# Performance work log

Hardware: AMD Instinct MI355X
Metric: run time of the kernel (lower is better)

The kernel has to match this reference:

```python
import jax, jax.numpy as jnp
import numpy as np

DIM = 1024
NUM_HEADS = 16
HEAD_DIM = DIM // NUM_HEADS
EPS = 1e-5


def layernorm(x, scale, bias):
    # LayerNorm over the last (head_dim) axis
    mu = jnp.mean(x, axis=-1, keepdims=True)
    var = jnp.var(x, axis=-1, keepdims=True)
    return (x - mu) * jax.lax.rsqrt(var + EPS) * scale + bias


def rope(q):
    # q: [B, H, S, Hd]; standard rotate-half RoPE over head_dim
    S, Hd = q.shape[-2], q.shape[-1]
    inv_freq = 1.0 / (10000.0 ** (jnp.arange(0, Hd, 2, dtype=jnp.float32) / Hd))
    ang = jnp.arange(S, dtype=jnp.float32)[:, None] * inv_freq  # [S, Hd/2]
    cos, sin = jnp.cos(ang), jnp.sin(ang)
    q1, q2 = jnp.split(q, 2, axis=-1)
    return jnp.concatenate([q1 * cos - q2 * sin, q1 * sin + q2 * cos], axis=-1)


def setup_inputs() -> dict:
    key = jax.random.key(0)
    ks = jax.random.split(key, 8)
    B, S, S_ctx = 4, 2048, 2048
    s = 0.02
    return {
        "x": jax.random.normal(ks[0], (B, S, DIM), dtype=jnp.float32),
        "context": jax.random.normal(ks[1], (B, S_ctx, DIM), dtype=jnp.float32),
        "q_w": jax.random.normal(ks[2], (DIM, DIM), dtype=jnp.float32) * s,
        "kv_w": jax.random.normal(ks[3], (DIM, 2 * DIM), dtype=jnp.float32) * s,
        "qn_scale": jnp.ones((HEAD_DIM,), jnp.float32),
        "qn_bias": jnp.zeros((HEAD_DIM,), jnp.float32),
        "kn_scale": jnp.ones((HEAD_DIM,), jnp.float32),
        "kn_bias": jnp.zeros((HEAD_DIM,), jnp.float32),
        "proj_w": jax.random.normal(ks[4], (DIM, DIM), dtype=jnp.float32) * s,
        "proj_b": jnp.zeros((DIM,), jnp.float32),
    }


def reference(x, context, q_w, kv_w, qn_scale, qn_bias, kn_scale, kn_bias, proj_w, proj_b):
    B, S, C = x.shape
    S_ctx = context.shape[1]
    H, Hd = NUM_HEADS, HEAD_DIM
    # projections (no bias: qkv_bias=False)
    q = (x @ q_w).reshape(B, S, H, Hd).transpose(0, 2, 1, 3)        # [B,H,S,Hd]
    kv = (context @ kv_w).reshape(B, S_ctx, 2, H, Hd)
    k = kv[:, :, 0].transpose(0, 2, 1, 3)                           # [B,H,Sc,Hd]
    v = kv[:, :, 1].transpose(0, 2, 1, 3)
    # per-head LayerNorm on q and k
    q = layernorm(q, qn_scale, qn_bias)
    k = layernorm(k, kn_scale, kn_bias)
    # RoPE on q only (as in the original forward)
    q = rope(q)
    # SDPA (eval path: no mask, no dropout)
    scale = 1.0 / jnp.sqrt(jnp.float32(Hd))
    logits = jnp.einsum("bhsd,bhtd->bhst", q, k) * scale
    attn = jax.nn.softmax(logits, axis=-1)
    out = jnp.einsum("bhst,bhtd->bhsd", attn, v)                    # [B,H,S,Hd]
    out = out.transpose(0, 2, 1, 3).reshape(B, S, C)
    return out @ proj_w + proj_b
```

## Files before the change

kernel.cpp:

```cpp
#include <hip/hip_runtime.h>
#include <hip/hip_bf16.h>


typedef short bf16x8 __attribute__((ext_vector_type(8)));
typedef float f32x4 __attribute__((ext_vector_type(4)));

__device__ __forceinline__ short f2s(float f) {
    __hip_bfloat16 h = __float2bfloat16(f);
    return __builtin_bit_cast(short, h);
}

__device__ __forceinline__ f32x4 mfma16(bf16x8 a, bf16x8 b, f32x4 c) {
    return __builtin_amdgcn_mfma_f32_16x16x32_bf16(a, b, c, 0, 0, 0);
}

__device__ __forceinline__ void gload16(short* lds, const short* g) {
    __builtin_amdgcn_global_load_lds((const __attribute__((address_space(1))) void*)g,
                                     (__attribute__((address_space(3))) void*)lds,
                                     16, 0, 0);
}

__device__ __forceinline__ void drain_barrier() {
    asm volatile("s_waitcnt vmcnt(0) lgkmcnt(0)" ::: "memory");
    __syncthreads();
}

__device__ __forceinline__ unsigned int fbits(float f) {
    return __builtin_bit_cast(unsigned int, f);
}

__global__ __launch_bounds__(256) void conv_to_bf16(const float* __restrict__ x,
                                                    const float* __restrict__ ctx,
                                                    short* __restrict__ xb,
                                                    short* __restrict__ cb) {
    const size_t NV = 2097152;
    size_t i = (size_t)blockIdx.x * 256 + threadIdx.x;
    const float4* src = (i < NV) ? (const float4*)x : (const float4*)ctx;
    short* dst = (i < NV) ? xb : cb;
    size_t idx = (i < NV) ? i : i - NV;
    float4 v = src[idx];
    short4 o;
    o.x = f2s(v.x); o.y = f2s(v.y); o.z = f2s(v.z); o.w = f2s(v.w);
    ((short4*)dst)[idx] = o;
}

__global__ __launch_bounds__(256) void transpose_weights(
    const float* __restrict__ q_w, const float* __restrict__ kv_w,
    const float* __restrict__ proj_w,
    short* __restrict__ WqT, short* __restrict__ WkvT, short* __restrict__ WpT) {
    __shared__ float t[32][33];
    const float* src; short* dst; int ld, coff;
    switch (blockIdx.z) {
        case 0:  src = q_w;    dst = WqT;                 ld = 1024; coff = 0;    break;
        case 1:  src = kv_w;   dst = WkvT;                ld = 2048; coff = 0;    break;
        case 2:  src = kv_w;   dst = WkvT + 1024 * 1024;  ld = 2048; coff = 1024; break;
        default: src = proj_w; dst = WpT;                 ld = 1024; coff = 0;    break;
    }
    int n0 = blockIdx.x * 32, k0 = blockIdx.y * 32;
    int tx = threadIdx.x & 31, ty = threadIdx.x >> 5;
    #pragma unroll
    for (int j = 0; j < 32; j += 8)
        t[ty + j][tx] = src[(size_t)(k0 + ty + j) * ld + coff + n0 + tx];
    __syncthreads();
    #pragma unroll
    for (int j = 0; j < 32; j += 8)
        dst[(size_t)(n0 + ty + j) * 1024 + k0 + tx] = f2s(t[tx][ty + j]);
}

template <int MODE>
__global__ __launch_bounds__(256, 3) void gemm128(
    const short* __restrict__ A,
    const short* __restrict__ Bt,
    const short* __restrict__ A2,
    const short* __restrict__ Bt2,
    const float* __restrict__ qn_scale, const float* __restrict__ qn_bias,
    const float* __restrict__ kn_scale, const float* __restrict__ kn_bias,
    short* __restrict__ outQ, short* __restrict__ outK, short* __restrict__ outV,
    float* __restrict__ outF, const float* __restrict__ bias_vec) {
    __shared__ short smem[24576];
    const int tid = threadIdx.x;
    const int w = tid >> 6, lane = tid & 63, quad = lane >> 4, l15 = lane & 15;
    const int wr = w & 1, wc = w >> 1;
    const int m0 = blockIdx.x * 128;

    int n0;
    bool qpath = true, vpath = false;
    const short *Ab, *Bb;
    const float *lns = qn_scale, *lnb = qn_bias;
    if constexpr (MODE == 3) {
        const int y = blockIdx.y;
        qpath = (y < 8);
        n0 = qpath ? y * 128 : (y - 8) * 128;
        Ab = qpath ? A : A2;
        Bb = qpath ? Bt : Bt2;
        lns = qpath ? qn_scale : kn_scale;
        lnb = qpath ? qn_bias : kn_bias;
        vpath = (!qpath) && (n0 >= 1024);
    } else {
        n0 = blockIdx.y * 128;
        Ab = A; Bb = Bt;
    }

    const int srow = lane >> 2, slot = lane & 3;
    const int kslot = (slot ^ ((srow >> 1) & 3)) * 8;
    const short* Ag0 = Ab + (size_t)(m0 + w * 32 + srow) * 1024 + kslot;
    const short* Ag1 = Ag0 + (size_t)16 * 1024;
    const short* Bg0 = Bb + (size_t)(n0 + w * 32 + srow) * 1024 + kslot;
    const short* Bg1 = Bg0 + (size_t)16 * 1024;
    short* Al = smem + w * 1024;
    short* Bl = smem + 4096 + w * 1024;

    f32x4 acc[4][4];
    #pragma unroll
    for (int r = 0; r < 4; r++)
        #pragma unroll
        for (int c = 0; c < 4; c++) acc[r][c] = f32x4{0.f, 0.f, 0.f, 0.f};

    const int rsw = (l15 >> 1) & 3;
    const int rch = (quad ^ rsw) * 8;

    gload16(Al,              Ag0);
    gload16(Al + 512,        Ag1);
    gload16(Bl,              Bg0);
    gload16(Bl + 512,        Bg1);
    gload16(Al + 8192,       Ag0 + 32);
    gload16(Al + 8192 + 512, Ag1 + 32);
    gload16(Bl + 8192,       Bg0 + 32);
    gload16(Bl + 8192 + 512, Bg1 + 32);
    asm volatile("s_waitcnt vmcnt(4) lgkmcnt(0)" ::: "memory");
    __builtin_amdgcn_s_barrier();

    int curo = 0;
    int pfo = 16384;
    #pragma unroll 1
    for (int t = 0; t < 32; t++) {
        if (t < 30) {
            const int k0 = (t + 2) * 32;
            gload16(Al + pfo,       Ag0 + k0);
            gload16(Al + pfo + 512, Ag1 + k0);
            gload16(Bl + pfo,       Bg0 + k0);
            gload16(Bl + pfo + 512, Bg1 + k0);
        }
        bf16x8 af[4], bfr[4];
        #pragma unroll
        for (int rt = 0; rt < 4; rt++)
            af[rt] = *(const bf16x8*)(smem + curo + (wr * 64 + rt * 16 + l15) * 32 + rch);
        #pragma unroll
        for (int ct = 0; ct < 4; ct++)
            bfr[ct] = *(const bf16x8*)(smem + curo + 4096 + (wc * 64 + ct * 16 + l15) * 32 + rch);
        #pragma unroll
        for (int rt = 0; rt < 4; rt++)
            #pragma unroll
            for (int ct = 0; ct < 4; ct++)
                acc[rt][ct] = mfma16(af[rt], bfr[ct], acc[rt][ct]);
        if (t < 30) {
            asm volatile("s_waitcnt vmcnt(4) lgkmcnt(0)" ::: "memory");
        } else {
            asm volatile("s_waitcnt vmcnt(0) lgkmcnt(0)" ::: "memory");
        }
        __builtin_amdgcn_s_barrier();
        curo += 8192; if (curo == 24576) curo = 0;
        pfo  += 8192; if (pfo  == 24576) pfo  = 0;
    }

    if constexpr (MODE == 3) {
        if (!vpath) {
            #pragma unroll
            for (int rt = 0; rt < 4; rt++) {
                #pragma unroll
                for (int i = 0; i < 4; i++) {
                    float s = acc[rt][0][i] + acc[rt][1][i] + acc[rt][2][i] + acc[rt][3][i];
                    float q = acc[rt][0][i] * acc[rt][0][i] + acc[rt][1][i] * acc[rt][1][i] +
                              acc[rt][2][i] * acc[rt][2][i] + acc[rt][3][i] * acc[rt][3][i];
                    #pragma unroll
                    for (int off = 1; off < 16; off <<= 1) {
                        s += __shfl_xor(s, off, 64);
                        q += __shfl_xor(q, off, 64);
                    }
                    float mu = s * (1.f / 64.f);
                    float var = q * (1.f / 64.f) - mu * mu;
                    float rs = rsqrtf(var + 1e-5f);
                    float vals[4];
                    #pragma unroll
                    for (int ct = 0; ct < 4; ct++) {
                        int hd = ct * 16 + l15;
                        vals[ct] = (acc[rt][ct][i] - mu) * rs * lns[hd] + lnb[hd];
                    }
                    if (qpath) {
                        int sp = (m0 + wr * 64 + rt * 16 + quad * 4 + i) & 2047;
                        #pragma unroll
                        for (int ct = 0; ct < 2; ct++) {
                            int hd1 = ct * 16 + l15;
                            float ang = (float)sp * exp2f((float)hd1 * (-13.287712379549449f / 32.f));
                            float sn, cs;
                            sincosf(ang, &sn, &cs);
                            float v1 = vals[ct], v2 = vals[ct + 2];
                            vals[ct]     = v1 * cs - v2 * sn;
                            vals[ct + 2] = v1 * sn + v2 * cs;
                        }
                        #pragma unroll
                        for (int ct = 0; ct < 4; ct++) vals[ct] *= 0.1803368801f;
                    }
                    #pragma unroll
                    for (int ct = 0; ct < 4; ct++) acc[rt][ct][i] = vals[ct];
                }
            }
            drain_barrier();
            short* Csm = smem;
            #pragma unroll
            for (int rt = 0; rt < 4; rt++)
                #pragma unroll
                for (int ct = 0; ct < 4; ct++)
                    #pragma unroll
                    for (int i = 0; i < 4; i++)
                        Csm[(wr * 64 + rt * 16 + quad * 4 + i) * 132 + wc * 64 + ct * 16 + l15] =
                            f2s(acc[rt][ct][i]);
            drain_barrier();
            short* dst = qpath ? outQ : outK;
            #pragma unroll
            for (int it = 0; it < 8; it++) {
                int row = it * 16 + (tid >> 4);
                int chunk = tid & 15;
                bf16x8 v = *(const bf16x8*)(Csm + row * 132 + chunk * 8);
                int hh = ((n0 & 1023) >> 6) + (chunk >> 3);
                int m = m0 + row, b = m >> 11, sp = m & 2047;
                *(bf16x8*)(dst + ((size_t)(b * 16 + hh) * 2048 + sp) * 64 + (chunk & 7) * 8) = v;
            }
        } else {
            const int b = m0 >> 11, h = ((n0 - 1024) >> 6) + wc;
            const int sp = (m0 & 2047) + wr * 64 + quad * 4;
            #pragma unroll
            for (int rt = 0; rt < 4; rt++)
                #pragma unroll
                for (int ct = 0; ct < 4; ct++) {
                    short4 pk;
                    pk.x = f2s(acc[rt][ct][0]); pk.y = f2s(acc[rt][ct][1]);
                    pk.z = f2s(acc[rt][ct][2]); pk.w = f2s(acc[rt][ct][3]);
                    int hd = ct * 16 + l15;
                    *(short4*)(outV + ((size_t)(b * 16 + h) * 64 + hd) * 2048 + sp + rt * 16) = pk;
                }
        }
    } else {
        #pragma unroll
        for (int rt = 0; rt < 4; rt++)
            #pragma unroll
            for (int i = 0; i < 4; i++) {
                size_t m = m0 + wr * 64 + rt * 16 + quad * 4 + i;
                #pragma unroll
                for (int ct = 0; ct < 4; ct++) {
                    int n = n0 + wc * 64 + ct * 16 + l15;
                    outF[m * 1024 + n] = acc[rt][ct][i] + bias_vec[n];
                }
            }
    }
}

__global__ __launch_bounds__(256, 2) void attn_kernel(
    const short* __restrict__ Q,
    const short* __restrict__ K,
    const short* __restrict__ V,
    short* __restrict__ AO) {
    __shared__ short smem[8192 + 8192 + 2 * 4 * 32 * 72];
    const int tid = threadIdx.x;
    const int w = tid >> 6, lane = tid & 63, quad = lane >> 4, l15 = lane & 15;
    const int bh = blockIdx.x, qt = blockIdx.y;
    const short* Qb = Q + (size_t)bh * 2048 * 64;
    const short* Kb = K + (size_t)bh * 2048 * 64;
    const short* Vb = V + (size_t)bh * 64 * 2048;
    const int q0g[2] = {qt * 128 + w * 32, (qt + 8) * 128 + w * 32};

    const int srow = lane >> 2, slot = lane & 3;
    const int sw = (slot ^ ((srow >> 1) & 3)) * 8;
    const short* Kg = Kb + (size_t)(w * 16 + srow) * 64 + sw;
    const short* Vg = Vb + (size_t)(w * 16 + srow) * 2048 + sw;
    short* Kl0 = smem + w * 512;
    short* Vl0 = smem + 8192 + w * 512;

    bf16x8 bq[2][2][2];
    #pragma unroll
    for (int g = 0; g < 2; g++)
        #pragma unroll
        for (int nt = 0; nt < 2; nt++)
            #pragma unroll
            for (int ks = 0; ks < 2; ks++)
                bq[g][nt][ks] =
                    *(const bf16x8*)(Qb + (size_t)(q0g[g] + nt * 16 + l15) * 64 + ks * 32 + quad * 8);

    f32x4 acco[2][4][2];
    #pragma unroll
    for (int g = 0; g < 2; g++)
        #pragma unroll
        for (int ct = 0; ct < 4; ct++)
            #pragma unroll
            for (int nt = 0; nt < 2; nt++) acco[g][ct][nt] = f32x4{0.f, 0.f, 0.f, 0.f};
    float lsum[2][2] = {{0.f, 0.f}, {0.f, 0.f}};
    const int rsw = (l15 >> 1) & 3;
    const int rch = (quad ^ rsw) * 8;

    gload16(Kl0,        Kg);
    gload16(Kl0 + 2048, Kg + 32);
    gload16(Vl0,        Vg);
    gload16(Vl0 + 2048, Vg + 32);
    drain_barrier();

    #pragma unroll 1
    for (int t = 0; t < 32; t++) {
        const int cur = (t & 1) * 4096;
        if (t < 31) {
            const int nxt = 4096 - cur;
            const int sc = (t + 1) * 64;
            gload16(Kl0 + nxt,        Kg + sc * 64);
            gload16(Kl0 + nxt + 2048, Kg + sc * 64 + 32);
            gload16(Vl0 + nxt,        Vg + sc);
            gload16(Vl0 + nxt + 2048, Vg + sc + 32);
        }
        bf16x8 ak[4][2];
        #pragma unroll
        for (int mt = 0; mt < 4; mt++)
            #pragma unroll
            for (int ks = 0; ks < 2; ks++)
                ak[mt][ks] = *(const bf16x8*)(smem + cur + ks * 2048 + (mt * 16 + l15) * 32 + rch);

        #pragma unroll
        for (int g = 0; g < 2; g++) {
            short* Pw = smem + 16384 + g * 9216 + w * 2304;
            #pragma unroll
            for (int mt = 0; mt < 4; mt++) {
                #pragma unroll
                for (int nt = 0; nt < 2; nt++) {
                    f32x4 st = f32x4{0.f, 0.f, 0.f, 0.f};
                    st = mfma16(ak[mt][0], bq[g][nt][0], st);
                    st = mfma16(ak[mt][1], bq[g][nt][1], st);
                    float e0 = __builtin_amdgcn_exp2f(st[0]);
                    float e1 = __builtin_amdgcn_exp2f(st[1]);
                    float e2 = __builtin_amdgcn_exp2f(st[2]);
                    float e3 = __builtin_amdgcn_exp2f(st[3]);
                    lsum[g][nt] += (e0 + e1) + (e2 + e3);
                    unsigned int p01 = __builtin_amdgcn_perm(fbits(e1), fbits(e0), 0x07060302u);
                    unsigned int p23 = __builtin_amdgcn_perm(fbits(e3), fbits(e2), 0x07060302u);
                    uint2 pw;
                    pw.x = p01; pw.y = p23;
                    *(uint2*)(Pw + (nt * 16 + l15) * 72 + mt * 16 + quad * 4) = pw;
                }
            }
        }
        asm volatile("" ::: "memory");

        bf16x8 av[4][2];
        #pragma unroll
        for (int ct = 0; ct < 4; ct++)
            #pragma unroll
            for (int ks = 0; ks < 2; ks++)
                av[ct][ks] = *(const bf16x8*)(smem + 8192 + cur + ks * 2048 + (ct * 16 + l15) * 32 + rch);

        #pragma unroll
        for (int g = 0; g < 2; g++) {
            short* Pw = smem + 16384 + g * 9216 + w * 2304;
            bf16x8 bp[2][2];
            #pragma unroll
            for (int nt = 0; nt < 2; nt++)
                #pragma unroll
                for (int ks = 0; ks < 2; ks++)
                    bp[nt][ks] = *(const bf16x8*)(Pw + (nt * 16 + l15) * 72 + ks * 32 + quad * 8);
            #pragma unroll
            for (int ct = 0; ct < 4; ct++)
                #pragma unroll
                for (int nt = 0; nt < 2; nt++)
                    #pragma unroll
                    for (int ks = 0; ks < 2; ks++)
                        acco[g][ct][nt] = mfma16(av[ct][ks], bp[nt][ks], acco[g][ct][nt]);
        }
        drain_barrier();
    }

    #pragma unroll
    for (int g = 0; g < 2; g++)
        #pragma unroll
        for (int nt = 0; nt < 2; nt++) {
            lsum[g][nt] += __shfl_xor(lsum[g][nt], 16, 64);
            lsum[g][nt] += __shfl_xor(lsum[g][nt], 32, 64);
        }
    const int b = bh >> 4, h = bh & 15;
    #pragma unroll
    for (int g = 0; g < 2; g++)
        #pragma unroll
        for (int nt = 0; nt < 2; nt++) {
            float inv = 1.f / lsum[g][nt];
            int sq = q0g[g] + nt * 16 + l15;
            #pragma unroll
            for (int ct = 0; ct < 4; ct++) {
                short4 pk;
                pk.x = f2s(acco[g][ct][nt][0] * inv); pk.y = f2s(acco[g][ct][nt][1] * inv);
                pk.z = f2s(acco[g][ct][nt][2] * inv); pk.w = f2s(acco[g][ct][nt][3] * inv);
                *(short4*)(AO + ((size_t)b * 2048 + sq) * 1024 + h * 64 + ct * 16 + quad * 4) = pk;
            }
        }
}

extern "C" void kernel_launch(void* const* d_in, const int* in_sizes, int n_in,
                              void* d_out, int out_size, void* d_ws, size_t ws_size,
                              hipStream_t stream) {
    (void)in_sizes; (void)n_in; (void)out_size; (void)ws_size;
    const float* x      = (const float*)d_in[0];
    const float* ctx    = (const float*)d_in[1];
    const float* q_w    = (const float*)d_in[2];
    const float* kv_w   = (const float*)d_in[3];
    const float* qn_s   = (const float*)d_in[4];
    const float* qn_b   = (const float*)d_in[5];
    const float* kn_s   = (const float*)d_in[6];
    const float* kn_b   = (const float*)d_in[7];
    const float* proj_w = (const float*)d_in[8];
    const float* proj_b = (const float*)d_in[9];
    float* out = (float*)d_out;

    char* ws = (char*)d_ws;
    const size_t MB = 1024 * 1024;
    short* xb   = (short*)(ws + 0 * MB);
    short* cb   = (short*)(ws + 16 * MB);
    short* Qb   = (short*)(ws + 32 * MB);
    short* Kb   = (short*)(ws + 48 * MB);
    short* Vt   = (short*)(ws + 64 * MB);
    short* AO   = (short*)(ws + 80 * MB);
    short* WqT  = (short*)(ws + 96 * MB);
    short* WkvT = (short*)(ws + 98 * MB);
    short* WpT  = (short*)(ws + 102 * MB);

    conv_to_bf16<<<16384, 256, 0, stream>>>(x, ctx, xb, cb);
    transpose_weights<<<dim3(32, 32, 4), 256, 0, stream>>>(q_w, kv_w, proj_w, WqT, WkvT, WpT);
    gemm128<3><<<dim3(64, 24), 256, 0, stream>>>(xb, WqT, cb, WkvT, qn_s, qn_b, kn_s, kn_b,
                                                 Qb, Kb, Vt, nullptr, nullptr);
    attn_kernel<<<dim3(64, 8), 256, 0, stream>>>(Qb, Kb, Vt, AO);
    gemm128<2><<<dim3(64, 8), 256, 0, stream>>>(AO, WpT, nullptr, nullptr, nullptr, nullptr,
                                                nullptr, nullptr, nullptr, nullptr, nullptr,
                                                out, proj_b);
}
```

Before: 304.7 us.

## Split attention work across 8 waves of 32 queries each instead of 4 waves

The attention kernel now runs 512 threads (8 waves) per block, and each wave owns 32 query rows instead of two groups of 32. K/V staging is split so waves 0-3 load K tiles and waves 4-7 load V tiles, halving the global loads each wave issues. Per-wave registers (accumulators, Q fragments) shrink, which should allow more waves in flight and better latency hiding. In exchange, each block has more threads joining every barrier, and the launch bound of 4 blocks of 512 threads may force register spilling.

```diff
diff --git a/kernel.cpp b/kernel.cpp
--- a/kernel.cpp
+++ b/kernel.cpp
@@ -255,52 +255,48 @@
     }
 }
 
-__global__ __launch_bounds__(256, 2) void attn_kernel(
+__global__ __launch_bounds__(512, 4) void attn_kernel(
     const short* __restrict__ Q,
     const short* __restrict__ K,
     const short* __restrict__ V,
     short* __restrict__ AO) {
-    __shared__ short smem[8192 + 8192 + 2 * 4 * 32 * 72];
+    __shared__ short smem[8192 + 8192 + 8 * 32 * 72];
     const int tid = threadIdx.x;
     const int w = tid >> 6, lane = tid & 63, quad = lane >> 4, l15 = lane & 15;
     const int bh = blockIdx.x, qt = blockIdx.y;
     const short* Qb = Q + (size_t)bh * 2048 * 64;
     const short* Kb = K + (size_t)bh * 2048 * 64;
     const short* Vb = V + (size_t)bh * 64 * 2048;
-    const int q0g[2] = {qt * 128 + w * 32, (qt + 8) * 128 + w * 32};
+    short* Pw = smem + 16384 + w * 2304;
+    const int q0 = qt * 256 + w * 32;
 
     const int srow = lane >> 2, slot = lane & 3;
     const int sw = (slot ^ ((srow >> 1) & 3)) * 8;
-    const short* Kg = Kb + (size_t)(w * 16 + srow) * 64 + sw;
-    const short* Vg = Vb + (size_t)(w * 16 + srow) * 2048 + sw;
-    short* Kl0 = smem + w * 512;
-    short* Vl0 = smem + 8192 + w * 512;
-
-    bf16x8 bq[2][2][2];
-    #pragma unroll
-    for (int g = 0; g < 2; g++)
-        #pragma unroll
-        for (int nt = 0; nt < 2; nt++)
-            #pragma unroll
-            for (int ks = 0; ks < 2; ks++)
-                bq[g][nt][ks] =
-                    *(const bf16x8*)(Qb + (size_t)(q0g[g] + nt * 16 + l15) * 64 + ks * 32 + quad * 8);
-
-    f32x4 acco[2][4][2];
-    #pragma unroll
-    for (int g = 0; g < 2; g++)
-        #pragma unroll
-        for (int ct = 0; ct < 4; ct++)
-            #pragma unroll
-            for (int nt = 0; nt < 2; nt++) acco[g][ct][nt] = f32x4{0.f, 0.f, 0.f, 0.f};
-    float lsum[2][2] = {{0.f, 0.f}, {0.f, 0.f}};
+    const int ws = w & 3;
+    const bool kstager = (w < 4);
+    const short* Sg = kstager ? (Kb + (size_t)(ws * 16 + srow) * 64 + sw)
+                              : (Vb + (size_t)(ws * 16 + srow) * 2048 + sw);
+    short* Sl0 = smem + (kstager ? 0 : 8192) + ws * 512;
+    const int sstep = kstager ? 4096 : 64;
+
+    bf16x8 bq[2][2];
+    #pragma unroll
+    for (int nt = 0; nt < 2; nt++)
+        #pragma unroll
+        for (int ks = 0; ks < 2; ks++)
+            bq[nt][ks] = *(const bf16x8*)(Qb + (size_t)(q0 + nt * 16 + l15) * 64 + ks * 32 + quad * 8);
+
+    f32x4 acco[4][2];
+    #pragma unroll
+    for (int ct = 0; ct < 4; ct++)
+        #pragma unroll
+        for (int nt = 0; nt < 2; nt++) acco[ct][nt] = f32x4{0.f, 0.f, 0.f, 0.f};
+    float lsum[2] = {0.f, 0.f};
     const int rsw = (l15 >> 1) & 3;
     const int rch = (quad ^ rsw) * 8;
 
-    gload16(Kl0,        Kg);
-    gload16(Kl0 + 2048, Kg + 32);
-    gload16(Vl0,        Vg);
-    gload16(Vl0 + 2048, Vg + 32);
+    gload16(Sl0,        Sg);
+    gload16(Sl0 + 2048, Sg + 32);
     drain_barrier();
 
     #pragma unroll 1
@@ -308,11 +304,8 @@
         const int cur = (t & 1) * 4096;
         if (t < 31) {
             const int nxt = 4096 - cur;
-            const int sc = (t + 1) * 64;
-            gload16(Kl0 + nxt,        Kg + sc * 64);
-            gload16(Kl0 + nxt + 2048, Kg + sc * 64 + 32);
-            gload16(Vl0 + nxt,        Vg + sc);
-            gload16(Vl0 + nxt + 2048, Vg + sc + 32);
+            gload16(Sl0 + nxt,        Sg + (t + 1) * sstep);
+            gload16(Sl0 + nxt + 2048, Sg + (t + 1) * sstep + 32);
         }
         bf16x8 ak[4][2];
         #pragma unroll
@@ -322,26 +315,22 @@
                 ak[mt][ks] = *(const bf16x8*)(smem + cur + ks * 2048 + (mt * 16 + l15) * 32 + rch);
 
         #pragma unroll
-        for (int g = 0; g < 2; g++) {
-            short* Pw = smem + 16384 + g * 9216 + w * 2304;
-            #pragma unroll
-            for (int mt = 0; mt < 4; mt++) {
-                #pragma unroll
-                for (int nt = 0; nt < 2; nt++) {
-                    f32x4 st = f32x4{0.f, 0.f, 0.f, 0.f};
-                    st = mfma16(ak[mt][0], bq[g][nt][0], st);
-                    st = mfma16(ak[mt][1], bq[g][nt][1], st);
-                    float e0 = __builtin_amdgcn_exp2f(st[0]);
-                    float e1 = __builtin_amdgcn_exp2f(st[1]);
-                    float e2 = __builtin_amdgcn_exp2f(st[2]);
-                    float e3 = __builtin_amdgcn_exp2f(st[3]);
-                    lsum[g][nt] += (e0 + e1) + (e2 + e3);
-                    unsigned int p01 = __builtin_amdgcn_perm(fbits(e1), fbits(e0), 0x07060302u);
-                    unsigned int p23 = __builtin_amdgcn_perm(fbits(e3), fbits(e2), 0x07060302u);
-                    uint2 pw;
-                    pw.x = p01; pw.y = p23;
-                    *(uint2*)(Pw + (nt * 16 + l15) * 72 + mt * 16 + quad * 4) = pw;
-                }
+        for (int mt = 0; mt < 4; mt++) {
+            #pragma unroll
+            for (int nt = 0; nt < 2; nt++) {
+                f32x4 st = f32x4{0.f, 0.f, 0.f, 0.f};
+                st = mfma16(ak[mt][0], bq[nt][0], st);
+                st = mfma16(ak[mt][1], bq[nt][1], st);
+                float e0 = __builtin_amdgcn_exp2f(st[0]);
+                float e1 = __builtin_amdgcn_exp2f(st[1]);
+                float e2 = __builtin_amdgcn_exp2f(st[2]);
+                float e3 = __builtin_amdgcn_exp2f(st[3]);
+                lsum[nt] += (e0 + e1) + (e2 + e3);
+                unsigned int p01 = __builtin_amdgcn_perm(fbits(e1), fbits(e0), 0x07060302u);
+                unsigned int p23 = __builtin_amdgcn_perm(fbits(e3), fbits(e2), 0x07060302u);
+                uint2 pw;
+                pw.x = p01; pw.y = p23;
+                *(uint2*)(Pw + (nt * 16 + l15) * 72 + mt * 16 + quad * 4) = pw;
             }
         }
         asm volatile("" ::: "memory");
@@ -353,48 +342,40 @@
             for (int ks = 0; ks < 2; ks++)
                 av[ct][ks] = *(const bf16x8*)(smem + 8192 + cur + ks * 2048 + (ct * 16 + l15) * 32 + rch);
 
-        #pragma unroll
-        for (int g = 0; g < 2; g++) {
-            short* Pw = smem + 16384 + g * 9216 + w * 2304;
-            bf16x8 bp[2][2];
+        bf16x8 bp[2][2];
+        #pragma unroll
+        for (int nt = 0; nt < 2; nt++)
+            #pragma unroll
+            for (int ks = 0; ks < 2; ks++)
+                bp[nt][ks] = *(const bf16x8*)(Pw + (nt * 16 + l15) * 72 + ks * 32 + quad * 8);
+        #pragma unroll
+        for (int ct = 0; ct < 4; ct++)
             #pragma unroll
             for (int nt = 0; nt < 2; nt++)
                 #pragma unroll
                 for (int ks = 0; ks < 2; ks++)
-                    bp[nt][ks] = *(const bf16x8*)(Pw + (nt * 16 + l15) * 72 + ks * 32 + quad * 8);
-            #pragma unroll
-            for (int ct = 0; ct < 4; ct++)
-                #pragma unroll
-                for (int nt = 0; nt < 2; nt++)
-                    #pragma unroll
-                    for (int ks = 0; ks < 2; ks++)
-                        acco[g][ct][nt] = mfma16(av[ct][ks], bp[nt][ks], acco[g][ct][nt]);
-        }
+                    acco[ct][nt] = mfma16(av[ct][ks], bp[nt][ks], acco[ct][nt]);
         drain_barrier();
     }
 
     #pragma unroll
-    for (int g = 0; g < 2; g++)
-        #pragma unroll
-        for (int nt = 0; nt < 2; nt++) {
-            lsum[g][nt] += __shfl_xor(lsum[g][nt], 16, 64);
-            lsum[g][nt] += __shfl_xor(lsum[g][nt], 32, 64);
-        }
+    for (int nt = 0; nt < 2; nt++) {
+        lsum[nt] += __shfl_xor(lsum[nt], 16, 64);
+        lsum[nt] += __shfl_xor(lsum[nt], 32, 64);
+    }
     const int b = bh >> 4, h = bh & 15;
     #pragma unroll
-    for (int g = 0; g < 2; g++)
-        #pragma unroll
-        for (int nt = 0; nt < 2; nt++) {
-            float inv = 1.f / lsum[g][nt];
-            int sq = q0g[g] + nt * 16 + l15;
-            #pragma unroll
-            for (int ct = 0; ct < 4; ct++) {
-                short4 pk;
-                pk.x = f2s(acco[g][ct][nt][0] * inv); pk.y = f2s(acco[g][ct][nt][1] * inv);
-                pk.z = f2s(acco[g][ct][nt][2] * inv); pk.w = f2s(acco[g][ct][nt][3] * inv);
-                *(short4*)(AO + ((size_t)b * 2048 + sq) * 1024 + h * 64 + ct * 16 + quad * 4) = pk;
-            }
-        }
+    for (int nt = 0; nt < 2; nt++) {
+        float inv = 1.f / lsum[nt];
+        int sq = q0 + nt * 16 + l15;
+        #pragma unroll
+        for (int ct = 0; ct < 4; ct++) {
+            short4 pk;
+            pk.x = f2s(acco[ct][nt][0] * inv); pk.y = f2s(acco[ct][nt][1] * inv);
+            pk.z = f2s(acco[ct][nt][2] * inv); pk.w = f2s(acco[ct][nt][3] * inv);
+            *(short4*)(AO + ((size_t)b * 2048 + sq) * 1024 + h * 64 + ct * 16 + quad * 4) = pk;
+        }
+    }
 }
 
 extern "C" void kernel_launch(void* const* d_in, const int* in_sizes, int n_in,
@@ -429,7 +410,7 @@
     transpose_weights<<<dim3(32, 32, 4), 256, 0, stream>>>(q_w, kv_w, proj_w, WqT, WkvT, WpT);
     gemm128<3><<<dim3(64, 24), 256, 0, stream>>>(xb, WqT, cb, WkvT, qn_s, qn_b, kn_s, kn_b,
                                                  Qb, Kb, Vt, nullptr, nullptr);
-    attn_kernel<<<dim3(64, 8), 256, 0, stream>>>(Qb, Kb, Vt, AO);
+    attn_kernel<<<dim3(64, 8), 512, 0, stream>>>(Qb, Kb, Vt, AO);
     gemm128<2><<<dim3(64, 8), 256, 0, stream>>>(AO, WpT, nullptr, nullptr, nullptr, nullptr,
                                                 nullptr, nullptr, nullptr, nullptr, nullptr,
                                                 out, proj_b);
```

New measurement: 299.6 us. No clear change (-1.7%).
